# Optimization experiments

Measured on AMD Instinct MI355X. Metric: run time of the kernel, lower is better.

The kernel has to match this reference:

```python
import jax, jax.numpy as jnp
import numpy as np

D = 256; HEADS = 8; DH = D // HEADS; NLEV = 1; NPTS = 4; NLAYERS = 6
N = 4; LQ = 900; H_ = 128; W_ = 128; LEN = H_ * W_; DFF = 4 * D; LNEPS = 1e-5


def _ln(x, g, b):
    m = jnp.mean(x, -1, keepdims=True)
    v = jnp.mean((x - m) ** 2, -1, keepdims=True)
    return (x - m) * jax.lax.rsqrt(v + LNEPS) * g + b


def _inv_sigmoid(x, eps=1e-5):
    x = jnp.clip(x, 0.0, 1.0)
    return jnp.log(jnp.clip(x, eps, None) / jnp.clip(1.0 - x, eps, None))


def _bilinear(v, loc):
    # v: (N,HEADS,LEN,DH) row-major HxW grid per head; loc: (N,LQ,HEADS,NPTS,2) normalized [0,1]
    # grid_sample(align_corners=False, padding_mode='zeros') semantics
    x = loc[..., 0] * W_ - 0.5
    y = loc[..., 1] * H_ - 0.5
    x0 = jnp.floor(x); y0 = jnp.floor(y)
    wx = x - x0; wy = y - y0
    x0i = x0.astype(jnp.int32); y0i = y0.astype(jnp.int32)

    def gather(xi, yi):
        valid = ((xi >= 0) & (xi < W_) & (yi >= 0) & (yi < H_)).astype(v.dtype)
        idx = jnp.clip(yi, 0, H_ - 1) * W_ + jnp.clip(xi, 0, W_ - 1)
        idx = idx.transpose(0, 2, 1, 3).reshape(N, HEADS, LQ * NPTS)
        g = jnp.take_along_axis(v, idx[..., None], axis=2).reshape(N, HEADS, LQ, NPTS, DH)
        return g * valid.transpose(0, 2, 1, 3)[..., None]

    def w(a):
        return a.transpose(0, 2, 1, 3)[..., None]

    return (gather(x0i, y0i) * w((1 - wx) * (1 - wy))
            + gather(x0i + 1, y0i) * w(wx * (1 - wy))
            + gather(x0i, y0i + 1) * w((1 - wx) * wy)
            + gather(x0i + 1, y0i + 1) * w(wx * wy))  # (N,HEADS,LQ,NPTS,DH)


def _forward(tgt, reference_points, src, src_valid_ratios, query_pos,
             Wo, bo, Wa, ba, Wv, bv, Wout, bout, g1, b1, Wfc, bfc, Wproj, bproj, g2, b2,
             Wb1, bb1, Wb2, bb2, Wb3, bb3, src_padding_mask):
    output = tgt
    ref = reference_points
    inter, inter_ref = [], []
    vr4 = jnp.concatenate([src_valid_ratios, src_valid_ratios], -1)  # (N,NLEV,4)
    for l in range(NLAYERS):
        ref_in = ref[:, :, None] * vr4[:, None]  # (N,LQ,NLEV,4)
        q = output + query_pos
        # MSDeformAttn
        value = src @ Wv[l] + bv[l]
        value = jnp.where(src_padding_mask[..., None], 0.0, value)
        value = value.reshape(N, LEN, HEADS, DH).transpose(0, 2, 1, 3)  # (N,HEADS,LEN,DH)
        off = (q @ Wo[l] + bo[l]).reshape(N, LQ, HEADS, NLEV, NPTS, 2)
        aw = jax.nn.softmax((q @ Wa[l] + ba[l]).reshape(N, LQ, HEADS, NLEV * NPTS), -1)
        aw = aw.reshape(N, LQ, HEADS, NLEV, NPTS)
        # 4-dim reference points: center + half-wh scaled offsets
        loc = ref_in[:, :, None, :, None, :2] + off / NPTS * ref_in[:, :, None, :, None, 2:] * 0.5
        samp = _bilinear(value, loc[:, :, :, 0])  # single level
        attn = jnp.einsum('nhqpd,nqhp->nqhd', samp, aw[:, :, :, 0]).reshape(N, LQ, D)
        attn = attn @ Wout[l] + bout[l]
        # residual + LN + MLP (the 'gelu' slot is actually ReLU in the source)
        x = _ln(output + attn, g1[l], b1[l])
        x = _ln(x + jax.nn.relu(x @ Wfc[l] + bfc[l]) @ Wproj[l] + bproj[l], g2[l], b2[l])
        # bbox refinement
        tmp = jax.nn.relu(jax.nn.relu(x @ Wb1[l] + bb1[l]) @ Wb2[l] + bb2[l]) @ Wb3[l] + bb3[l]
        ref = jax.lax.stop_gradient(jax.nn.sigmoid(tmp + _inv_sigmoid(ref)))
        output = x
        inter.append(output)
        inter_ref.append(ref)
    return jnp.stack(inter), jnp.stack(inter_ref)


def setup_inputs():
    key = jax.random.key(0)
    ks = jax.random.split(key, 16)
    rn = lambda k, s, sc=0.02: jax.random.normal(k, s, jnp.float32) * sc
    P2 = HEADS * NLEV * NPTS * 2
    P1 = HEADS * NLEV * NPTS
    return dict(
        tgt=jax.random.normal(ks[0], (N, LQ, D), jnp.float32),
        reference_points=jax.random.uniform(ks[1], (N, LQ, 4), jnp.float32, 0.1, 0.9),
        src=jax.random.normal(ks[2], (N, LEN, D), jnp.float32),
        src_valid_ratios=jnp.ones((N, NLEV, 2), jnp.float32),
        query_pos=jax.random.normal(ks[3], (N, LQ, D), jnp.float32),
        Wo=rn(ks[4], (NLAYERS, D, P2)), bo=rn(ks[5], (NLAYERS, P2), 0.1),
        Wa=rn(ks[6], (NLAYERS, D, P1)), ba=jnp.zeros((NLAYERS, P1), jnp.float32),
        Wv=rn(ks[7], (NLAYERS, D, D)), bv=jnp.zeros((NLAYERS, D), jnp.float32),
        Wout=rn(ks[8], (NLAYERS, D, D)), bout=jnp.zeros((NLAYERS, D), jnp.float32),
        g1=jnp.ones((NLAYERS, D), jnp.float32), b1=jnp.zeros((NLAYERS, D), jnp.float32),
        Wfc=rn(ks[9], (NLAYERS, D, DFF)), bfc=jnp.zeros((NLAYERS, DFF), jnp.float32),
        Wproj=rn(ks[10], (NLAYERS, DFF, D)), bproj=jnp.zeros((NLAYERS, D), jnp.float32),
        g2=jnp.ones((NLAYERS, D), jnp.float32), b2=jnp.zeros((NLAYERS, D), jnp.float32),
        Wb1=rn(ks[11], (NLAYERS, D, D)), bb1=jnp.zeros((NLAYERS, D), jnp.float32),
        Wb2=rn(ks[12], (NLAYERS, D, D)), bb2=jnp.zeros((NLAYERS, D), jnp.float32),
        Wb3=rn(ks[13], (NLAYERS, D, 4)), bb3=jnp.zeros((NLAYERS, 4), jnp.float32),
        src_spatial_shapes=jnp.array([[H_, W_]], jnp.int32),
        src_level_start_index=jnp.array([0], jnp.int32),
        src_padding_mask=jnp.zeros((N, LEN), bool),
    )


def reference(tgt, reference_points, src, src_valid_ratios, query_pos,
              Wo, bo, Wa, ba, Wv, bv, Wout, bout, g1, b1, Wfc, bfc, Wproj, bproj, g2, b2,
              Wb1, bb1, Wb2, bb2, Wb3, bb3, src_spatial_shapes, src_level_start_index,
              src_padding_mask):
    return _forward(tgt, reference_points, src, src_valid_ratios, query_pos,
                    Wo, bo, Wa, ba, Wv, bv, Wout, bout, g1, b1, Wfc, bfc, Wproj, bproj, g2, b2,
                    Wb1, bb1, Wb2, bb2, Wb3, bb3, src_padding_mask)
```

## Files before the change

### kernel.cpp

```cpp
#include <hip/hip_runtime.h>
#include <hip/hip_bf16.h>
#include <math.h>

constexpr int N_    = 4;
constexpr int LQ    = 900;
constexpr int D     = 256;
constexpr int HEADS = 8;
constexpr int DH    = 32;
constexpr int NPTS  = 4;
constexpr int LEN   = 16384;
constexpr int H_    = 128;
constexpr int W_    = 128;
constexpr int DFF   = 1024;
constexpr int NLAYERS = 6;
constexpr int MQ    = N_ * LQ;
constexpr int MV    = N_ * LEN;
constexpr int MB    = (MQ + 63) / 64;
constexpr int VBLK  = (D / 128) * (MV / 128);
constexpr int QBLK  = 2 * MB;

typedef __attribute__((ext_vector_type(8))) short bf16x8;
typedef __attribute__((ext_vector_type(4))) float f32x4;

static __device__ __forceinline__ unsigned short f2bf(float v) {
    __hip_bfloat16 h = __float2bfloat16(v);
    return *(unsigned short*)&h;
}
static __device__ __forceinline__ float bf2f(unsigned short u) {
    __hip_bfloat16 h = *(__hip_bfloat16*)&u;
    return __bfloat162float(h);
}
static __device__ __forceinline__ bf16x8 pack8(const float* a, const float* b4) {
    union { bf16x8 v; unsigned short u[8]; } o;
    o.u[0] = f2bf(a[0]); o.u[1] = f2bf(a[1]); o.u[2] = f2bf(a[2]); o.u[3] = f2bf(a[3]);
    o.u[4] = f2bf(b4[0]); o.u[5] = f2bf(b4[1]); o.u[6] = f2bf(b4[2]); o.u[7] = f2bf(b4[3]);
    return o.v;
}

static __device__ __forceinline__ void gload_lds16(const void* gaddr, void* laddr) {
    __builtin_amdgcn_global_load_lds(
        (const __attribute__((address_space(1))) unsigned int*)gaddr,
        (__attribute__((address_space(3))) unsigned int*)laddr,
        16, 0, 0);
}

__global__ __launch_bounds__(256) void cvt_bf16_kernel(
    const float* __restrict__ in, unsigned short* __restrict__ out, int n8)
{
    int i = blockIdx.x * 256 + threadIdx.x;
    if (i >= n8) return;
    float4 a = ((const float4*)in)[i * 2];
    float4 b = ((const float4*)in)[i * 2 + 1];
    float af[4] = {a.x, a.y, a.z, a.w}, bff[4] = {b.x, b.y, b.z, b.w};
    *(bf16x8*)(out + (size_t)i * 8) = pack8(af, bff);
}

__global__ __launch_bounds__(256) void wt_cvt4_kernel(
    const float* __restrict__ W0, const float* __restrict__ W1,
    const float* __restrict__ W2, const float* __restrict__ W3,
    unsigned short* __restrict__ T0, unsigned short* __restrict__ T1,
    unsigned short* __restrict__ T2, unsigned short* __restrict__ T3)
{
    int i = blockIdx.x * 256 + threadIdx.x;
    if (i >= NLAYERS * D * D) return;
    int k = i & (D - 1);
    int n = (i >> 8) & (D - 1);
    int l = i >> 16;
    size_t si = (size_t)l * D * D + (size_t)k * D + n;
    T0[i] = f2bf(W0[si]);
    T1[i] = f2bf(W1[si]);
    T2[i] = f2bf(W2[si]);
    T3[i] = f2bf(W3[si]);
}

__global__ __launch_bounds__(256) void wt_cvt_kernel(
    const float* __restrict__ W, unsigned short* __restrict__ WT,
    int K, int Nr, int Npad, int total)
{
    int i = blockIdx.x * 256 + threadIdx.x;
    if (i >= total) return;
    int k = i % K;
    int n = (i / K) % Npad;
    int l = i / (K * Npad);
    WT[i] = (n < Nr) ? f2bf(W[((size_t)l * K + k) * Nr + n]) : (unsigned short)0;
}

__global__ __launch_bounds__(256) void woat_kernel(
    const float* __restrict__ Wo, const float* __restrict__ Wa,
    unsigned short* __restrict__ WoaT)
{
    int i = blockIdx.x * 256 + threadIdx.x;
    if (i >= NLAYERS * 128 * D) return;
    int k = i % D;
    int n = (i / D) & 127;
    int l = i / (D * 128);
    float v = 0.f;
    if (n < 64)      v = Wo[((size_t)l * D + k) * 64 + n];
    else if (n < 96) v = Wa[((size_t)l * D + k) * 32 + (n - 64)];
    WoaT[i] = f2bf(v);
}

__global__ __launch_bounds__(256) void bias_concat_kernel(
    const float* __restrict__ bo, const float* __restrict__ ba, float* __restrict__ boa)
{
    int i = blockIdx.x * 256 + threadIdx.x;
    if (i >= NLAYERS * 128) return;
    int n = i & 127;
    int l = i >> 7;
    float v = 0.f;
    if (n < 64)      v = bo[l * 64 + n];
    else if (n < 96) v = ba[l * 32 + (n - 64)];
    boa[i] = v;
}

__global__ __launch_bounds__(256) void fused_vq_kernel(
    const unsigned short* __restrict__ A, const unsigned short* __restrict__ Bt,
    const float* __restrict__ bias, const unsigned char* __restrict__ mask,
    unsigned short* __restrict__ C,
    const float* __restrict__ Aq, const float* __restrict__ A2q,
    const unsigned short* __restrict__ Btq, const float* __restrict__ biasq,
    float* __restrict__ Cq)
{
    __shared__ unsigned short Asm[128 * 64];
    __shared__ unsigned short Bsm[128 * 64];

    const int bid  = blockIdx.x;
    const int tid  = threadIdx.x;
    const int wave = tid >> 6;
    const int lane = tid & 63;
    const int lg   = lane >> 4;
    const int lr   = lane & 15;

    if (bid < VBLK) {
        const int y  = (bid >> 4) * 8 + (bid & 7);
        const int x  = (bid >> 3) & 1;
        const int m0 = y * 128;
        const int n0 = x * 128;
        const int wr = wave >> 1;
        const int wc = wave & 1;

        f32x4 acc[4][4];
#pragma unroll
        for (int i = 0; i < 4; ++i)
#pragma unroll
            for (int j = 0; j < 4; ++j) acc[i][j] = (f32x4){0.f, 0.f, 0.f, 0.f};

        for (int k0 = 0; k0 < D; k0 += 64) {
#pragma unroll
            for (int it = 0; it < 4; ++it) {
                int c   = tid + it * 256;
                int row = c >> 3;
                int kch = (c & 7) ^ (row & 7);
                unsigned ldsoff = (unsigned)(it * 256 + wave * 64) * 16;
                gload_lds16(A  + (size_t)(m0 + row) * D + k0 + kch * 8, (char*)Asm + ldsoff);
                gload_lds16(Bt + (size_t)(n0 + row) * D + k0 + kch * 8, (char*)Bsm + ldsoff);
            }
            __syncthreads();

            bf16x8 af[4][2], bfr[4][2];
#pragma unroll
            for (int i = 0; i < 4; ++i) {
#pragma unroll
                for (int kk = 0; kk < 2; ++kk) {
                    int arow = wr * 64 + i * 16 + lr;
                    af[i][kk]  = *(const bf16x8*)((char*)Asm + arow * 128 + 16 * ((kk * 4 + lg) ^ (arow & 7)));
                    int brow = wc * 64 + i * 16 + lr;
                    bfr[i][kk] = *(const bf16x8*)((char*)Bsm + brow * 128 + 16 * ((kk * 4 + lg) ^ (brow & 7)));
                }
            }
#pragma unroll
            for (int kk = 0; kk < 2; ++kk)
#pragma unroll
                for (int i = 0; i < 4; ++i)
#pragma unroll
                    for (int j = 0; j < 4; ++j)
                        acc[i][j] = __builtin_amdgcn_mfma_f32_16x16x32_bf16(
                            af[i][kk], bfr[j][kk], acc[i][j], 0, 0, 0);
            __syncthreads();
        }

#pragma unroll
        for (int i = 0; i < 4; ++i) {
            int mbase = m0 + wr * 64 + i * 16 + lg * 4;
#pragma unroll
            for (int j = 0; j < 4; ++j) {
                int n = n0 + wc * 64 + j * 16 + lr;
                float bn = bias[n];
#pragma unroll
                for (int r = 0; r < 4; ++r) {
                    int m = mbase + r;
                    float v = acc[i][j][r] + bn;
                    if (mask[m]) v = 0.f;
                    C[(size_t)m * D + n] = f2bf(v);
                }
            }
        }
    } else {
        const int qb = bid - VBLK;
        const int n0 = (qb & 1) * 64;
        const int m0 = (qb >> 1) * 64;
        const int wr = wave >> 1;
        const int wc = wave & 1;

        f32x4 acc[2][2];
#pragma unroll
        for (int i = 0; i < 2; ++i)
#pragma unroll
            for (int j = 0; j < 2; ++j) acc[i][j] = (f32x4){0.f, 0.f, 0.f, 0.f};

        for (int k0 = 0; k0 < D; k0 += 64) {
#pragma unroll
            for (int it = 0; it < 2; ++it) {
                int c   = tid + it * 256;
                int row = c >> 3;
                int kc  = c & 7;
                int kch = kc ^ (row & 7);
                unsigned ldsoff = (unsigned)(it * 256 + wave * 64) * 16;
                gload_lds16(Btq + (size_t)(n0 + row) * D + k0 + kch * 8, (char*)Bsm + ldsoff);
                int gm = m0 + row;
                bf16x8 v = (bf16x8){0,0,0,0,0,0,0,0};
                if (gm < MQ) {
                    const float* ap = Aq  + (size_t)gm * D + k0 + kc * 8;
                    const float* qp = A2q + (size_t)gm * D + k0 + kc * 8;
                    float4 a = *(const float4*)ap;
                    float4 b = *(const float4*)(ap + 4);
                    float4 qa = *(const float4*)qp;
                    float4 qb4 = *(const float4*)(qp + 4);
                    a.x += qa.x; a.y += qa.y; a.z += qa.z; a.w += qa.w;
                    b.x += qb4.x; b.y += qb4.y; b.z += qb4.z; b.w += qb4.w;
                    float af_[4] = {a.x, a.y, a.z, a.w}, bf_[4] = {b.x, b.y, b.z, b.w};
                    v = pack8(af_, bf_);
                }
                *(bf16x8*)((char*)Asm + row * 128 + 16 * (kc ^ (row & 7))) = v;
            }
            __syncthreads();

            bf16x8 af[2][2], bfr[2][2];
#pragma unroll
            for (int i = 0; i < 2; ++i) {
#pragma unroll
                for (int kk = 0; kk < 2; ++kk) {
                    int arow = wr * 32 + i * 16 + lr;
                    af[i][kk]  = *(const bf16x8*)((char*)Asm + arow * 128 + 16 * ((kk * 4 + lg) ^ (arow & 7)));
                    int brow = wc * 32 + i * 16 + lr;
                    bfr[i][kk] = *(const bf16x8*)((char*)Bsm + brow * 128 + 16 * ((kk * 4 + lg) ^ (brow & 7)));
                }
            }
#pragma unroll
            for (int kk = 0; kk < 2; ++kk)
#pragma unroll
                for (int i = 0; i < 2; ++i)
#pragma unroll
                    for (int j = 0; j < 2; ++j)
                        acc[i][j] = __builtin_amdgcn_mfma_f32_16x16x32_bf16(
                            af[i][kk], bfr[j][kk], acc[i][j], 0, 0, 0);
            __syncthreads();
        }

#pragma unroll
        for (int i = 0; i < 2; ++i) {
            int mbase = m0 + wr * 32 + i * 16 + lg * 4;
#pragma unroll
            for (int j = 0; j < 2; ++j) {
                int n = n0 + wc * 32 + j * 16 + lr;
                if (n >= 96) continue;
                float bn = biasq[n];
#pragma unroll
                for (int r = 0; r < 4; ++r) {
                    int m = mbase + r;
                    if (m >= MQ) continue;
                    Cq[(size_t)m * 96 + n] = acc[i][j][r] + bn;
                }
            }
        }
    }
}

template<bool ABF16, bool RELU, bool OUTBF16>
__global__ __launch_bounds__(256) void gemm_q_mfma(
    const void* __restrict__ Av,
    const unsigned short* __restrict__ Bt, const float* __restrict__ bias,
    void* __restrict__ Cv, int M, int Nreal, int K)
{
    __shared__ unsigned short Asm[64 * 64];
    __shared__ unsigned short Bsm[64 * 64];

    const int tid  = threadIdx.x;
    const int m0   = blockIdx.y * 64;
    const int n0   = blockIdx.x * 64;
    const int wave = tid >> 6;
    const int lane = tid & 63;
    const int wr   = wave >> 1;
    const int wc   = wave & 1;
    const int lg   = lane >> 4;
    const int lr   = lane & 15;

    f32x4 acc[2][2];
#pragma unroll
    for (int i = 0; i < 2; ++i)
#pragma unroll
        for (int j = 0; j < 2; ++j) acc[i][j] = (f32x4){0.f, 0.f, 0.f, 0.f};

    for (int k0 = 0; k0 < K; k0 += 64) {
#pragma unroll
        for (int it = 0; it < 2; ++it) {
            int c   = tid + it * 256;
            int row = c >> 3;
            int kch = (c & 7) ^ (row & 7);
            unsigned ldsoff = (unsigned)(it * 256 + wave * 64) * 16;
            gload_lds16(Bt + (size_t)(n0 + row) * K + k0 + kch * 8, (char*)Bsm + ldsoff);
            if (ABF16) {
                gload_lds16((const unsigned short*)Av + (size_t)(m0 + row) * K + k0 + kch * 8,
                            (char*)Asm + ldsoff);
            } else {
                int kc = c & 7;
                int gm = m0 + row;
                bf16x8 v = (bf16x8){0,0,0,0,0,0,0,0};
                if (gm < M) {
                    const float* ap = (const float*)Av + (size_t)gm * K + k0 + kc * 8;
                    float4 a = *(const float4*)ap;
                    float4 b = *(const float4*)(ap + 4);
                    float af_[4] = {a.x, a.y, a.z, a.w}, bf_[4] = {b.x, b.y, b.z, b.w};
                    v = pack8(af_, bf_);
                }
                *(bf16x8*)((char*)Asm + row * 128 + 16 * (kc ^ (row & 7))) = v;
            }
        }
        __syncthreads();

        bf16x8 af[2][2], bfr[2][2];
#pragma unroll
        for (int i = 0; i < 2; ++i) {
#pragma unroll
            for (int kk = 0; kk < 2; ++kk) {
                int arow = wr * 32 + i * 16 + lr;
                af[i][kk]  = *(const bf16x8*)((char*)Asm + arow * 128 + 16 * ((kk * 4 + lg) ^ (arow & 7)));
                int brow = wc * 32 + i * 16 + lr;
                bfr[i][kk] = *(const bf16x8*)((char*)Bsm + brow * 128 + 16 * ((kk * 4 + lg) ^ (brow & 7)));
            }
        }
#pragma unroll
        for (int kk = 0; kk < 2; ++kk)
#pragma unroll
            for (int i = 0; i < 2; ++i)
#pragma unroll
                for (int j = 0; j < 2; ++j)
                    acc[i][j] = __builtin_amdgcn_mfma_f32_16x16x32_bf16(
                        af[i][kk], bfr[j][kk], acc[i][j], 0, 0, 0);
        __syncthreads();
    }

#pragma unroll
    for (int i = 0; i < 2; ++i) {
        int mbase = m0 + wr * 32 + i * 16 + lg * 4;
#pragma unroll
        for (int j = 0; j < 2; ++j) {
            int n = n0 + wc * 32 + j * 16 + lr;
            if (n >= Nreal) continue;
            float bn = bias[n];
#pragma unroll
            for (int r = 0; r < 4; ++r) {
                int m = mbase + r;
                if (m >= M) continue;
                float v = acc[i][j][r] + bn;
                if (RELU) v = fmaxf(v, 0.f);
                if (OUTBF16) ((unsigned short*)Cv)[(size_t)m * Nreal + n] = f2bf(v);
                else         ((float*)Cv)[(size_t)m * Nreal + n] = v;
            }
        }
    }
}

__global__ __launch_bounds__(256) void ln_kernel(
    const float* __restrict__ a, const float* __restrict__ b,
    const float* __restrict__ g, const float* __restrict__ be,
    float* __restrict__ out, unsigned short* __restrict__ outh)
{
    int row  = blockIdx.x * 4 + (threadIdx.x >> 6);
    int lane = threadIdx.x & 63;
    if (row >= MQ) return;

    const float4 va = *(const float4*)(a + (size_t)row * D + lane * 4);
    const float4 vb = *(const float4*)(b + (size_t)row * D + lane * 4);
    float x[4] = { va.x + vb.x, va.y + vb.y, va.z + vb.z, va.w + vb.w };

    float s = x[0] + x[1] + x[2] + x[3];
    float s2 = x[0]*x[0] + x[1]*x[1] + x[2]*x[2] + x[3]*x[3];
#pragma unroll
    for (int o = 32; o >= 1; o >>= 1) {
        s  += __shfl_xor(s,  o);
        s2 += __shfl_xor(s2, o);
    }
    float mean = s * (1.f / D);
    float var  = s2 * (1.f / D) - mean * mean;
    float rinv = rsqrtf(var + 1e-5f);

    float4 vg = *(const float4*)(g  + lane * 4);
    float4 vbe = *(const float4*)(be + lane * 4);
    float4 vo;
    vo.x = (x[0] - mean) * rinv * vg.x + vbe.x;
    vo.y = (x[1] - mean) * rinv * vg.y + vbe.y;
    vo.z = (x[2] - mean) * rinv * vg.z + vbe.z;
    vo.w = (x[3] - mean) * rinv * vg.w + vbe.w;
    *(float4*)(out + (size_t)row * D + lane * 4) = vo;

    ushort4 ho;
    ho.x = f2bf(vo.x); ho.y = f2bf(vo.y); ho.z = f2bf(vo.z); ho.w = f2bf(vo.w);
    *(ushort4*)(outh + (size_t)row * D + lane * 4) = ho;
}

__global__ __launch_bounds__(256) void sample_kernel(
    const unsigned short* __restrict__ value, const float* __restrict__ qoa,
    const float* __restrict__ ref_prev, const float* __restrict__ svr,
    float* __restrict__ attn)
{
    int nq = blockIdx.x;
    int h  = threadIdx.x >> 5;
    int dh = threadIdx.x & 31;
    int n  = nq / LQ;

    float vr0 = svr[n * 2 + 0], vr1 = svr[n * 2 + 1];
    float r0 = ref_prev[nq * 4 + 0] * vr0;
    float r1 = ref_prev[nq * 4 + 1] * vr1;
    float r2 = ref_prev[nq * 4 + 2] * vr0;
    float r3 = ref_prev[nq * 4 + 3] * vr1;

    const float* qrow = qoa + (size_t)nq * 96;

    float lgt[4];
    float mx = -1e30f;
#pragma unroll
    for (int p = 0; p < 4; ++p) {
        lgt[p] = qrow[64 + h * 4 + p];
        mx = fmaxf(mx, lgt[p]);
    }
    float ssum = 0.f;
#pragma unroll
    for (int p = 0; p < 4; ++p) { lgt[p] = expf(lgt[p] - mx); ssum += lgt[p]; }
    float sinv = 1.f / ssum;

    const unsigned short* vbase = value + (size_t)n * LEN * D + h * DH + dh;
    float acc = 0.f;

#pragma unroll
    for (int p = 0; p < NPTS; ++p) {
        float ox = qrow[h * 8 + p * 2 + 0];
        float oy = qrow[h * 8 + p * 2 + 1];
        float lx = r0 + ox * (1.f / NPTS) * r2 * 0.5f;
        float ly = r1 + oy * (1.f / NPTS) * r3 * 0.5f;
        float w  = lgt[p] * sinv;

        float x = lx * W_ - 0.5f;
        float y = ly * H_ - 0.5f;
        x = fminf(fmaxf(x, -1e4f), 1e4f);
        y = fminf(fmaxf(y, -1e4f), 1e4f);
        float x0f = floorf(x), y0f = floorf(y);
        float wx = x - x0f, wy = y - y0f;
        int x0 = (int)x0f, y0 = (int)y0f;

        float v00 = 0.f, v10 = 0.f, v01 = 0.f, v11 = 0.f;
        bool xin0 = (x0 >= 0 && x0 < W_);
        bool xin1 = (x0 + 1 >= 0 && x0 + 1 < W_);
        bool yin0 = (y0 >= 0 && y0 < H_);
        bool yin1 = (y0 + 1 >= 0 && y0 + 1 < H_);
        if (xin0 && yin0) v00 = bf2f(vbase[(size_t)(y0 * W_ + x0) * D]);
        if (xin1 && yin0) v10 = bf2f(vbase[(size_t)(y0 * W_ + x0 + 1) * D]);
        if (xin0 && yin1) v01 = bf2f(vbase[(size_t)((y0 + 1) * W_ + x0) * D]);
        if (xin1 && yin1) v11 = bf2f(vbase[(size_t)((y0 + 1) * W_ + x0 + 1) * D]);

        float bil = v00 * (1.f - wx) * (1.f - wy)
                  + v10 * wx * (1.f - wy)
                  + v01 * (1.f - wx) * wy
                  + v11 * wx * wy;
        acc += w * bil;
    }
    attn[(size_t)nq * D + h * DH + dh] = acc;
}

__global__ __launch_bounds__(256) void bbox_kernel(
    const unsigned short* __restrict__ t2, const float* __restrict__ Wb3,
    const float* __restrict__ bb3, const float* __restrict__ ref_prev,
    float* __restrict__ ref_out)
{
    int row  = blockIdx.x * 4 + (threadIdx.x >> 6);
    int lane = threadIdx.x & 63;
    if (row >= MQ) return;

    float acc0 = 0.f, acc1 = 0.f, acc2 = 0.f, acc3 = 0.f;
    const unsigned short* tp = t2 + (size_t)row * D;
#pragma unroll
    for (int kk = 0; kk < D / 64; ++kk) {
        int k = lane + kk * 64;
        float tv = bf2f(tp[k]);
        const float4 wrow = *(const float4*)(Wb3 + (size_t)k * 4);
        acc0 = fmaf(tv, wrow.x, acc0);
        acc1 = fmaf(tv, wrow.y, acc1);
        acc2 = fmaf(tv, wrow.z, acc2);
        acc3 = fmaf(tv, wrow.w, acc3);
    }
#pragma unroll
    for (int o = 32; o >= 1; o >>= 1) {
        acc0 += __shfl_xor(acc0, o);
        acc1 += __shfl_xor(acc1, o);
        acc2 += __shfl_xor(acc2, o);
        acc3 += __shfl_xor(acc3, o);
    }
    if (lane == 0) {
        float t3[4] = { acc0 + bb3[0], acc1 + bb3[1], acc2 + bb3[2], acc3 + bb3[3] };
#pragma unroll
        for (int c = 0; c < 4; ++c) {
            float rp = ref_prev[(size_t)row * 4 + c];
            float xc = fminf(fmaxf(rp, 0.f), 1.f);
            float invsig = logf(fmaxf(xc, 1e-5f) / fmaxf(1.f - xc, 1e-5f));
            float sarg = t3[c] + invsig;
            ref_out[(size_t)row * 4 + c] = 1.f / (1.f + expf(-sarg));
        }
    }
}

extern "C" void kernel_launch(void* const* d_in, const int* in_sizes, int n_in,
                              void* d_out, int out_size, void* d_ws, size_t ws_size,
                              hipStream_t stream)
{
    const float* tgt    = (const float*)d_in[0];
    const float* refpts = (const float*)d_in[1];
    const float* src    = (const float*)d_in[2];
    const float* svr    = (const float*)d_in[3];
    const float* qpos   = (const float*)d_in[4];
    const float* Wo     = (const float*)d_in[5];
    const float* bo     = (const float*)d_in[6];
    const float* Wa     = (const float*)d_in[7];
    const float* ba     = (const float*)d_in[8];
    const float* Wv     = (const float*)d_in[9];
    const float* bv     = (const float*)d_in[10];
    const float* Wout   = (const float*)d_in[11];
    const float* bout   = (const float*)d_in[12];
    const float* g1     = (const float*)d_in[13];
    const float* b1     = (const float*)d_in[14];
    const float* Wfc    = (const float*)d_in[15];
    const float* bfc    = (const float*)d_in[16];
    const float* Wproj  = (const float*)d_in[17];
    const float* bproj  = (const float*)d_in[18];
    const float* g2     = (const float*)d_in[19];
    const float* b2     = (const float*)d_in[20];
    const float* Wb1    = (const float*)d_in[21];
    const float* bb1    = (const float*)d_in[22];
    const float* Wb2    = (const float*)d_in[23];
    const float* bb2    = (const float*)d_in[24];
    const float* Wb3    = (const float*)d_in[25];
    const float* bb3    = (const float*)d_in[26];
    const unsigned char* mask = (const unsigned char*)d_in[29];

    float* outp  = (float*)d_out;
    float* inter     = outp;
    float* inter_ref = outp + (size_t)NLAYERS * MQ * D;

    char* wsb = (char*)d_ws;
    unsigned short* value    = (unsigned short*)wsb;  wsb += (size_t)MV * D * 2;
    unsigned short* src_bf16 = (unsigned short*)wsb;  wsb += (size_t)MV * D * 2;
    unsigned short* WvT      = (unsigned short*)wsb;  wsb += (size_t)NLAYERS * D * D * 2;
    unsigned short* WoaT     = (unsigned short*)wsb;  wsb += (size_t)NLAYERS * 128 * D * 2;
    unsigned short* WoutT    = (unsigned short*)wsb;  wsb += (size_t)NLAYERS * D * D * 2;
    unsigned short* WfcT     = (unsigned short*)wsb;  wsb += (size_t)NLAYERS * DFF * D * 2;
    unsigned short* WprojT   = (unsigned short*)wsb;  wsb += (size_t)NLAYERS * D * DFF * 2;
    unsigned short* Wb1T     = (unsigned short*)wsb;  wsb += (size_t)NLAYERS * D * D * 2;
    unsigned short* Wb2T     = (unsigned short*)wsb;  wsb += (size_t)NLAYERS * D * D * 2;
    unsigned short* hmlp     = (unsigned short*)wsb;  wsb += (size_t)MQ * DFF * 2;
    unsigned short* t1b      = (unsigned short*)wsb;  wsb += (size_t)MQ * D * 2;
    unsigned short* t2b      = (unsigned short*)wsb;  wsb += (size_t)MQ * D * 2;
    unsigned short* x1h      = (unsigned short*)wsb;  wsb += (size_t)MQ * D * 2;
    unsigned short* x2h      = (unsigned short*)wsb;  wsb += (size_t)MQ * D * 2;
    float* boa   = (float*)wsb;        wsb += (size_t)NLAYERS * 128 * 4;
    float* ws    = (float*)wsb;
    float* qoab  = ws;                 size_t o = (size_t)MQ * 96;
    float* attnb = ws + o;             o += (size_t)MQ * D;
    float* tmpb  = ws + o;             o += (size_t)MQ * D;
    float* x1b   = ws + o;             o += (size_t)MQ * D;

    cvt_bf16_kernel<<<(MV * D / 8 + 255) / 256, 256, 0, stream>>>(src, src_bf16, MV * D / 8);
    {
        int t = NLAYERS * D * D;
        wt_cvt4_kernel<<<(t + 255) / 256, 256, 0, stream>>>(
            Wv, Wout, Wb1, Wb2, WvT, WoutT, Wb1T, Wb2T);
        t = NLAYERS * DFF * D;
        wt_cvt_kernel<<<(t + 255) / 256, 256, 0, stream>>>(Wfc,   WfcT,   D,   DFF, DFF, t);
        wt_cvt_kernel<<<(t + 255) / 256, 256, 0, stream>>>(Wproj, WprojT, DFF, D,   D,   t);
        t = NLAYERS * 128 * D;
        woat_kernel<<<(t + 255) / 256, 256, 0, stream>>>(Wo, Wa, WoaT);
        bias_concat_kernel<<<(NLAYERS * 128 + 255) / 256, 256, 0, stream>>>(bo, ba, boa);
    }

    for (int l = 0; l < NLAYERS; ++l) {
        const float* out_prev = (l == 0) ? tgt    : inter     + (size_t)(l - 1) * MQ * D;
        const float* ref_prev = (l == 0) ? refpts : inter_ref + (size_t)(l - 1) * MQ * 4;
        float* inter_l     = inter     + (size_t)l * MQ * D;
        float* inter_ref_l = inter_ref + (size_t)l * MQ * 4;

        fused_vq_kernel<<<VBLK + QBLK, 256, 0, stream>>>(
            src_bf16, WvT + (size_t)l * D * D, bv + (size_t)l * D, mask, value,
            out_prev, qpos, WoaT + (size_t)l * 128 * D, boa + (size_t)l * 128, qoab);

        sample_kernel<<<MQ, 256, 0, stream>>>(value, qoab, ref_prev, svr, attnb);

        gemm_q_mfma<false,false,false><<<dim3(4, MB), 256, 0, stream>>>(
            attnb, WoutT + (size_t)l * D * D, bout + (size_t)l * D, tmpb, MQ, D, D);

        ln_kernel<<<MQ / 4, 256, 0, stream>>>(
            out_prev, tmpb, g1 + (size_t)l * D, b1 + (size_t)l * D, x1b, x1h);

        gemm_q_mfma<true,true,true><<<dim3(DFF / 64, MB), 256, 0, stream>>>(
            x1h, WfcT + (size_t)l * DFF * D, bfc + (size_t)l * DFF, hmlp, MQ, DFF, D);

        gemm_q_mfma<true,false,false><<<dim3(4, MB), 256, 0, stream>>>(
            hmlp, WprojT + (size_t)l * D * DFF, bproj + (size_t)l * D, tmpb, MQ, D, DFF);

        ln_kernel<<<MQ / 4, 256, 0, stream>>>(
            x1b, tmpb, g2 + (size_t)l * D, b2 + (size_t)l * D, inter_l, x2h);

        gemm_q_mfma<true,true,true><<<dim3(4, MB), 256, 0, stream>>>(
            x2h, Wb1T + (size_t)l * D * D, bb1 + (size_t)l * D, t1b, MQ, D, D);

        gemm_q_mfma<true,true,true><<<dim3(4, MB), 256, 0, stream>>>(
            t1b, Wb2T + (size_t)l * D * D, bb2 + (size_t)l * D, t2b, MQ, D, D);

        bbox_kernel<<<MQ / 4, 256, 0, stream>>>(
            t2b, Wb3 + (size_t)l * D * 4, bb3 + (size_t)l * 4, ref_prev, inter_ref_l);
    }
}
```

Baseline: 624.7 us.

## Fuse next layer's value/query projections with bbox MLP first GEMM

Moves the per-layer value and query-offset projection for layer l+1 into the same launch as layer l's first bbox-MLP GEMM, adding extra blocks to the fused kernel. The first layer's projection is hoisted before the loop. This cuts one kernel launch per layer and lets the small bbox GEMM fill the GPU alongside the large value GEMM, removing a serialization point. Buffers value and qoab are overwritten earlier, which is safe only because the current layer's sample kernel has already consumed them.

```diff
diff --git a/kernel.cpp b/kernel.cpp
--- a/kernel.cpp
+++ b/kernel.cpp
@@ -18,6 +18,7 @@
 constexpr int MB    = (MQ + 63) / 64;
 constexpr int VBLK  = (D / 128) * (MV / 128);
 constexpr int QBLK  = 2 * MB;
+constexpr int BBLK  = 4 * MB;
 
 typedef __attribute__((ext_vector_type(8))) short bf16x8;
 typedef __attribute__((ext_vector_type(4))) float f32x4;
@@ -113,13 +114,16 @@
     boa[i] = v;
 }
 
+template<bool HAS_B1>
 __global__ __launch_bounds__(256) void fused_vq_kernel(
     const unsigned short* __restrict__ A, const unsigned short* __restrict__ Bt,
     const float* __restrict__ bias, const unsigned char* __restrict__ mask,
     unsigned short* __restrict__ C,
     const float* __restrict__ Aq, const float* __restrict__ A2q,
     const unsigned short* __restrict__ Btq, const float* __restrict__ biasq,
-    float* __restrict__ Cq)
+    float* __restrict__ Cq,
+    const unsigned short* __restrict__ Ab1, const unsigned short* __restrict__ Btb1,
+    const float* __restrict__ biasb1, unsigned short* __restrict__ Cb1)
 {
     __shared__ unsigned short Asm[128 * 64];
     __shared__ unsigned short Bsm[128 * 64];
@@ -195,7 +199,7 @@
                 }
             }
         }
-    } else {
+    } else if (bid < VBLK + QBLK) {
         const int qb = bid - VBLK;
         const int n0 = (qb & 1) * 64;
         const int m0 = (qb >> 1) * 64;
@@ -270,6 +274,68 @@
                     int m = mbase + r;
                     if (m >= MQ) continue;
                     Cq[(size_t)m * 96 + n] = acc[i][j][r] + bn;
+                }
+            }
+        }
+    } else if (HAS_B1) {
+        const int bb = bid - VBLK - QBLK;
+        const int n0 = (bb & 3) * 64;
+        const int m0 = (bb >> 2) * 64;
+        const int wr = wave >> 1;
+        const int wc = wave & 1;
+
+        f32x4 acc[2][2];
+#pragma unroll
+        for (int i = 0; i < 2; ++i)
+#pragma unroll
+            for (int j = 0; j < 2; ++j) acc[i][j] = (f32x4){0.f, 0.f, 0.f, 0.f};
+
+        for (int k0 = 0; k0 < D; k0 += 64) {
+#pragma unroll
+            for (int it = 0; it < 2; ++it) {
+                int c   = tid + it * 256;
+                int row = c >> 3;
+                int kch = (c & 7) ^ (row & 7);
+                unsigned ldsoff = (unsigned)(it * 256 + wave * 64) * 16;
+                gload_lds16(Btb1 + (size_t)(n0 + row) * D + k0 + kch * 8, (char*)Bsm + ldsoff);
+                gload_lds16(Ab1  + (size_t)(m0 + row) * D + k0 + kch * 8, (char*)Asm + ldsoff);
+            }
+            __syncthreads();
+
+            bf16x8 af[2][2], bfr[2][2];
+#pragma unroll
+            for (int i = 0; i < 2; ++i) {
+#pragma unroll
+                for (int kk = 0; kk < 2; ++kk) {
+                    int arow = wr * 32 + i * 16 + lr;
+                    af[i][kk]  = *(const bf16x8*)((char*)Asm + arow * 128 + 16 * ((kk * 4 + lg) ^ (arow & 7)));
+                    int brow = wc * 32 + i * 16 + lr;
+                    bfr[i][kk] = *(const bf16x8*)((char*)Bsm + brow * 128 + 16 * ((kk * 4 + lg) ^ (brow & 7)));
+                }
+            }
+#pragma unroll
+            for (int kk = 0; kk < 2; ++kk)
+#pragma unroll
+                for (int i = 0; i < 2; ++i)
+#pragma unroll
+                    for (int j = 0; j < 2; ++j)
+                        acc[i][j] = __builtin_amdgcn_mfma_f32_16x16x32_bf16(
+                            af[i][kk], bfr[j][kk], acc[i][j], 0, 0, 0);
+            __syncthreads();
+        }
+
+#pragma unroll
+        for (int i = 0; i < 2; ++i) {
+            int mbase = m0 + wr * 32 + i * 16 + lg * 4;
+#pragma unroll
+            for (int j = 0; j < 2; ++j) {
+                int n = n0 + wc * 32 + j * 16 + lr;
+#pragma unroll
+                for (int r = 0; r < 4; ++r) {
+                    int m = mbase + r;
+                    if (m >= MQ) continue;
+                    float v = fmaxf(acc[i][j][r] + biasb1[n], 0.f);
+                    Cb1[(size_t)m * D + n] = f2bf(v);
                 }
             }
         }
@@ -590,16 +656,17 @@
         bias_concat_kernel<<<(NLAYERS * 128 + 255) / 256, 256, 0, stream>>>(bo, ba, boa);
     }
 
+    fused_vq_kernel<false><<<VBLK + QBLK, 256, 0, stream>>>(
+        src_bf16, WvT, bv, mask, value,
+        tgt, qpos, WoaT, boa, qoab,
+        nullptr, nullptr, nullptr, nullptr);
+
     for (int l = 0; l < NLAYERS; ++l) {
+        const float* ref_prev = (l == 0) ? refpts : inter_ref + (size_t)(l - 1) * MQ * 4;
         const float* out_prev = (l == 0) ? tgt    : inter     + (size_t)(l - 1) * MQ * D;
-        const float* ref_prev = (l == 0) ? refpts : inter_ref + (size_t)(l - 1) * MQ * 4;
         float* inter_l     = inter     + (size_t)l * MQ * D;
         float* inter_ref_l = inter_ref + (size_t)l * MQ * 4;
 
-        fused_vq_kernel<<<VBLK + QBLK, 256, 0, stream>>>(
-            src_bf16, WvT + (size_t)l * D * D, bv + (size_t)l * D, mask, value,
-            out_prev, qpos, WoaT + (size_t)l * 128 * D, boa + (size_t)l * 128, qoab);
-
         sample_kernel<<<MQ, 256, 0, stream>>>(value, qoab, ref_prev, svr, attnb);
 
         gemm_q_mfma<false,false,false><<<dim3(4, MB), 256, 0, stream>>>(
@@ -617,8 +684,15 @@
         ln_kernel<<<MQ / 4, 256, 0, stream>>>(
             x1b, tmpb, g2 + (size_t)l * D, b2 + (size_t)l * D, inter_l, x2h);
 
-        gemm_q_mfma<true,true,true><<<dim3(4, MB), 256, 0, stream>>>(
-            x2h, Wb1T + (size_t)l * D * D, bb1 + (size_t)l * D, t1b, MQ, D, D);
+        if (l < NLAYERS - 1) {
+            fused_vq_kernel<true><<<VBLK + QBLK + BBLK, 256, 0, stream>>>(
+                src_bf16, WvT + (size_t)(l + 1) * D * D, bv + (size_t)(l + 1) * D, mask, value,
+                inter_l, qpos, WoaT + (size_t)(l + 1) * 128 * D, boa + (size_t)(l + 1) * 128, qoab,
+                x2h, Wb1T + (size_t)l * D * D, bb1 + (size_t)l * D, t1b);
+        } else {
+            gemm_q_mfma<true,true,true><<<dim3(4, MB), 256, 0, stream>>>(
+                x2h, Wb1T + (size_t)l * D * D, bb1 + (size_t)l * D, t1b, MQ, D, D);
+        }
 
         gemm_q_mfma<true,true,true><<<dim3(4, MB), 256, 0, stream>>>(
             t1b, Wb2T + (size_t)l * D * D, bb2 + (size_t)l * D, t2b, MQ, D, D);
```

Result: faster. 597.1 us (-4.4%).
